# Performance work log

Hardware: AMD Instinct MI355X
Metric: run time of the kernel (lower is better)

The kernel has to match this reference:

```python
import jax, jax.numpy as jnp
import numpy as np
from jax import lax

RESO = 64
PAD = 0.1
PLANES = ('xz', 'xy', 'yz')
_AX = {'xz': (0, 2), 'xy': (0, 1), 'yz': (1, 2)}


def _normalize(p, plane):
    a, b = _AX[plane]
    xy = jnp.stack([p[..., a], p[..., b]], axis=-1)
    xy = (xy + 0.5) / (1.0 + PAD + 1e-6)
    return jnp.clip(xy, 0.0, 1.0 - 1e-6)


def _coord2index(xy):
    xi = (xy * RESO).astype(jnp.int32)
    return xi[..., 0] + RESO * xi[..., 1]  # [B,N]


def _scatter_mean(feat, idx):  # feat [B,N,C], idx [B,N] -> [B,RESO^2,C]
    R2 = RESO * RESO
    def one(f, i):
        s = jnp.zeros((R2, f.shape[-1]), f.dtype).at[i].add(f)
        cnt = jnp.zeros((R2,), f.dtype).at[i].add(1.0)
        return s / jnp.maximum(cnt, 1.0)[:, None]
    return jax.vmap(one)(feat, idx)


def _resblock(x, W0, b0, W1, b1, Ws):
    h = jax.nn.relu(x @ W0.T + b0)
    dx = jax.nn.relu(h @ W1.T + b1)
    return x @ Ws.T + dx


def _conv(x, W, b):
    y = lax.conv_general_dilated(x, W, (1, 1), 'SAME', dimension_numbers=('NCHW', 'OIHW', 'NCHW'))
    return y + b[None, :, None, None]


def _grid_sample_border(fea, grid):
    # fea [B,C,H,W], grid [B,N,2] with (x->W, y->H) in [-1,1]; bilinear, border padding, align_corners=False
    B, C, H, W = fea.shape
    x = jnp.clip(((grid[..., 0] + 1.0) * W - 1.0) * 0.5, 0.0, W - 1.0)
    y = jnp.clip(((grid[..., 1] + 1.0) * H - 1.0) * 0.5, 0.0, H - 1.0)
    x0 = jnp.floor(x); y0 = jnp.floor(y)
    wx = (x - x0)[:, None, :]; wy = (y - y0)[:, None, :]
    x0i = x0.astype(jnp.int32); y0i = y0.astype(jnp.int32)
    x1i = jnp.minimum(x0i + 1, W - 1); y1i = jnp.minimum(y0i + 1, H - 1)
    flat = fea.reshape(B, C, H * W)
    g = lambda yi, xi: jnp.take_along_axis(flat, (yi * W + xi)[:, None, :], axis=2)  # [B,C,N]
    return (g(y0i, x0i) * (1 - wx) * (1 - wy) + g(y0i, x1i) * wx * (1 - wy)
            + g(y1i, x0i) * (1 - wx) * wy + g(y1i, x1i) * wx * wy)


def setup_inputs() -> dict:
    key = jax.random.key(0)
    ks = jax.random.split(key, 16)
    B, N, Nq, H, F = 4, 30000, 30000, 64, 256
    nrm = lambda k, sh, s: jax.random.normal(k, sh, jnp.float32) * s
    return {
        'p': jax.random.uniform(ks[0], (B, N, 3), jnp.float32, -0.5, 0.5),
        'query': jax.random.uniform(ks[1], (B, Nq, 3), jnp.float32, 0.0, 1.0),
        'fc_pos_W': nrm(ks[2], (2 * H, 3), 0.3),
        'fc_pos_b': jnp.zeros((2 * H,), jnp.float32),
        'blk_fc0_W': nrm(ks[3], (3, H, 2 * H), 0.08),
        'blk_fc0_b': jnp.zeros((3, H), jnp.float32),
        'blk_fc1_W': nrm(ks[4], (3, H, H), 0.1),
        'blk_fc1_b': jnp.zeros((3, H), jnp.float32),
        'blk_sc_W': nrm(ks[5], (3, H, 2 * H), 0.08),
        'fc_c_W': nrm(ks[6], (F, H), 0.1),
        'fc_c_b': jnp.zeros((F,), jnp.float32),
        'conv1_W': nrm(ks[7], (F, F, 3, 3), 0.02),
        'conv1_b': jnp.zeros((F,), jnp.float32),
        'conv2_W': nrm(ks[8], (F, F, 3, 3), 0.02),
        'conv2_b': jnp.zeros((F,), jnp.float32),
    }


def reference(p, query, fc_pos_W, fc_pos_b, blk_fc0_W, blk_fc0_b, blk_fc1_W, blk_fc1_b, blk_sc_W, fc_c_W, fc_c_b, conv1_W, conv1_b, conv2_W, conv2_b):
    # point-wise MLP with local pooling (scatter_mean to xz bins, gather back)
    net = p @ fc_pos_W.T + fc_pos_b                  # [B,N,2H]
    net = _resblock(net, blk_fc0_W[0], blk_fc0_b[0], blk_fc1_W[0], blk_fc1_b[0], blk_sc_W[0])  # [B,N,H]
    idx_xz = _coord2index(_normalize(p, 'xz'))       # [B,N]
    for i in (1, 2):
        binmean = _scatter_mean(net, idx_xz)         # [B,R2,H]
        pooled = jnp.take_along_axis(binmean, idx_xz[..., None], axis=1)  # [B,N,H]
        net = jnp.concatenate([net, pooled], axis=-1)
        net = _resblock(net, blk_fc0_W[i], blk_fc0_b[i], blk_fc1_W[i], blk_fc1_b[i], blk_sc_W[i])
    c = net @ fc_c_W.T + fc_c_b                      # [B,N,F]

    B = p.shape[0]
    F = fc_c_W.shape[0]
    out = 0.0
    for plane in PLANES:
        idx = _coord2index(_normalize(p, plane))
        fea = _scatter_mean(c, idx)                  # [B,R2,F]
        fea = fea.transpose(0, 2, 1).reshape(B, F, RESO, RESO)  # H axis = coord1, W axis = coord0
        fea = jax.nn.relu(_conv(fea, conv1_W, conv1_b))
        fea = jax.nn.relu(_conv(fea, conv2_W, conv2_b))
        a, b = _AX[plane]
        grid = jnp.stack([query[..., a], query[..., b]], axis=-1) * 2.0 - 1.0
        out = out + _grid_sample_border(fea, grid)   # [B,F,Nq]
    return out.transpose(0, 2, 1)                    # [B,Nq,F]
```

## Files before the change

### kernel.cpp

```cpp
#include <hip/hip_runtime.h>

#define NPTS 30000
#define PSTR 30208
#define BB 4
#define R2 4096
#define NIMG 12

typedef __attribute__((ext_vector_type(8))) short short8;
typedef __attribute__((ext_vector_type(4))) float floatx4;

__device__ __forceinline__ ushort f2bf(float x){
    union { float f; unsigned u; } v; v.f = x;
    unsigned r = (v.u + 0x7fffu + ((v.u >> 16) & 1u)) >> 16;
    return (ushort)r;
}
__device__ __forceinline__ float bf2f(ushort u){
    union { unsigned u; float f; } v; v.u = ((unsigned)u) << 16; return v.f;
}
__device__ __forceinline__ int p64i(int k){ return (k & 3)*16 + (k >> 2); }

__device__ __forceinline__ int coord_bin(float v){
    float t = (v + 0.5f) / 1.100001f;
    t = fminf(fmaxf(t, 0.0f), 0.999999f);
    return (int)(t * 64.0f);
}

__device__ __forceinline__ void gl_lds16(const ushort* g, ushort* l){
    __builtin_amdgcn_global_load_lds(
        (const __attribute__((address_space(1))) void*)g,
        (__attribute__((address_space(3))) void*)l, 16, 0, 0);
}

__global__ void k_prep(const float* __restrict__ fc_pos_W, const float* __restrict__ fc_pos_b,
                       const float* __restrict__ blk0W, const float* __restrict__ blk1W,
                       const float* __restrict__ blkSW, const float* __restrict__ fccW,
                       const float* __restrict__ c1W, const float* __restrict__ c2W,
                       float* __restrict__ WposTp, float* __restrict__ bposP,
                       ushort* __restrict__ Wcat, ushort* __restrict__ W1p,
                       ushort* __restrict__ Wcp,
                       ushort* __restrict__ WB1, ushort* __restrict__ WB2){
    int t = blockIdx.x*256 + threadIdx.x;
    if (t < 384){ int d = t/128, s = t%128;
        int j = (s<64)? p64i(s) : 64 + p64i(s-64);
        WposTp[t] = fc_pos_W[j*3 + d]; return; }
    t -= 384;
    if (t < 128){ int j = (t<64)? p64i(t) : 64 + p64i(t-64);
        bposP[t] = fc_pos_b[j]; return; }
    t -= 128;
    if (t < 49152){
        int i = t/16384, r = t%16384, n = r/128, kp = r%128;
        int ci = (kp<64)? p64i(kp) : 64 + p64i(kp-64);
        float v = (n<64)? blk0W[(i*64+n)*128 + ci] : blkSW[(i*64+(n-64))*128 + ci];
        Wcat[t] = f2bf(v); return; }
    t -= 49152;
    if (t < 12288){
        int i = t/4096, r = t%4096, n = r/64, kp = r%64;
        W1p[t] = f2bf(blk1W[(i*64+n)*64 + p64i(kp)]); return; }
    t -= 12288;
    if (t < 16384){
        int n = t/64, kp = t%64;
        Wcp[t] = f2bf(fccW[n*64 + p64i(kp)]); return; }
    t -= 16384;
    if (t < 589824){
        int e = t & 7; int rest = t >> 3; int ko = rest & 255; int g5 = rest >> 8;
        int qq = g5 & 3; int kc = (g5 >> 2) & 1; int cc = (g5 >> 3) & 3; int tap = g5 >> 5;
        int kp = cc*64 + kc*32 + qq*8 + e;
        int ci = 64*(kp>>6) + p64i(kp & 63);
        WB1[t] = f2bf(c1W[(ko*256+ci)*9 + tap]); return; }
    t -= 589824;
    if (t < 589824){
        int e = t & 7; int rest = t >> 3; int ko = rest & 255; int g5 = rest >> 8;
        int qq = g5 & 3; int kc = (g5 >> 2) & 1; int cc = (g5 >> 3) & 3; int tap = g5 >> 5;
        int kp = cc*64 + kc*32 + qq*8 + e;
        WB2[t] = f2bf(c2W[(ko*256+kp)*9 + tap]); return; }
}

__global__ void k_net0(const float* __restrict__ p, const float* __restrict__ WposTp,
                       const float* __restrict__ bposP,
                       ushort* __restrict__ NET0, int* __restrict__ IDX){
    int pt = blockIdx.x*256 + threadIdx.x;
    int b = blockIdx.y;
    if (pt >= NPTS) return;
    const float* pp = p + ((long)b*NPTS + pt)*3;
    float p0 = pp[0], p1 = pp[1], p2 = pp[2];
    int c0 = coord_bin(p0), c1 = coord_bin(p1), c2 = coord_bin(p2);
    IDX[(0*BB + b)*NPTS + pt] = c0 + 64*c2;
    IDX[(1*BB + b)*NPTS + pt] = c0 + 64*c1;
    IDX[(2*BB + b)*NPTS + pt] = c1 + 64*c2;
    ushort* out = NET0 + ((long)b*PSTR + pt)*128;
    #pragma unroll
    for (int s = 0; s < 128; s += 4){
        ushort4 v;
        v.x = f2bf(bposP[s+0] + p0*WposTp[s+0] + p1*WposTp[128+s+0] + p2*WposTp[256+s+0]);
        v.y = f2bf(bposP[s+1] + p0*WposTp[s+1] + p1*WposTp[128+s+1] + p2*WposTp[256+s+1]);
        v.z = f2bf(bposP[s+2] + p0*WposTp[s+2] + p1*WposTp[128+s+2] + p2*WposTp[256+s+2]);
        v.w = f2bf(bposP[s+3] + p0*WposTp[s+3] + p1*WposTp[128+s+3] + p2*WposTp[256+s+3]);
        *(ushort4*)(out + s) = v;
    }
}

__global__ void k_qbin(const float* __restrict__ query, int* __restrict__ qIDX){
    int t = blockIdx.x*256 + threadIdx.x;
    if (t >= BB*NPTS) return;
    const float* qp = query + (long)t*3;
    int x = min((int)(fmaxf(qp[0], 0.0f)*16.0f), 15);
    int y = min((int)(fmaxf(qp[1], 0.0f)*16.0f), 15);
    int z = min((int)(fmaxf(qp[2], 0.0f)*16.0f), 15);
    qIDX[t] = (x<<8) | (y<<4) | z;
}

__global__ void k_hist(const int* __restrict__ IDX, int* __restrict__ hist, int n){
    int t = blockIdx.x*256 + threadIdx.x;
    if (t >= n) return;
    int img = t / NPTS;
    atomicAdd(&hist[img*R2 + IDX[t]], 1);
}

__global__ void k_scan(const int* __restrict__ hist, int* __restrict__ binStart,
                       int* __restrict__ cursor){
    __shared__ int sums[256];
    int img = blockIdx.x; int tid = threadIdx.x;
    int v[16]; int s = 0;
    const int* h = hist + img*R2 + tid*16;
    #pragma unroll
    for (int i=0;i<16;i++){ v[i] = s; s += h[i]; }
    sums[tid] = s;
    __syncthreads();
    for (int d=1; d<256; d<<=1){
        int t = (tid>=d)? sums[tid-d] : 0;
        __syncthreads();
        sums[tid] += t;
        __syncthreads();
    }
    int base = (tid==0)? 0 : sums[tid-1];
    int* bs = binStart + img*R2 + tid*16;
    int* cu = cursor  + img*R2 + tid*16;
    #pragma unroll
    for (int i=0;i<16;i++){ bs[i] = base + v[i]; cu[i] = base + v[i]; }
}

__global__ void k_mklist(const int* __restrict__ IDX, int* __restrict__ cursor,
                         int* __restrict__ plist, int n){
    int t = blockIdx.x*256 + threadIdx.x;
    if (t >= n) return;
    int img = t / NPTS; int pt = t - img*NPTS;
    int bin = IDX[t];
    int pos = atomicAdd(&cursor[img*R2 + bin], 1);
    plist[img*NPTS + pos] = pt;
}

__global__ void __launch_bounds__(256) k_res_mfma(
        const ushort* __restrict__ X1, const ushort* __restrict__ X2, int s1, int s2,
        const ushort* __restrict__ Wcat, const float* __restrict__ b0,
        const ushort* __restrict__ W1p, const float* __restrict__ b1,
        ushort* __restrict__ Y){
    __shared__ __align__(16) ushort lds[4][64*72];
    int tid = threadIdx.x, lane = tid & 63, w = tid >> 6;
    int m16 = lane & 15, q = lane >> 4;
    int b = blockIdx.y;
    int pt0 = blockIdx.x*256 + w*64;
    const ushort* x1 = X1 + (long)b*PSTR*s1;
    const ushort* x2 = X2 + (long)b*PSTR*s2;
    floatx4 accH[4][4], accS[4][4];
    #pragma unroll
    for (int nt=0; nt<4; nt++){
        float bv = b0[nt*16 + m16];
        #pragma unroll
        for (int mt=0; mt<4; mt++){
            floatx4 t = {bv,bv,bv,bv}; accH[mt][nt] = t;
            floatx4 z = {0.f,0.f,0.f,0.f}; accS[mt][nt] = z;
        }
    }
    #pragma unroll
    for (int kk=0; kk<4; kk++){
        const ushort* xs = (kk<2)? x1 : x2;
        int st = (kk<2)? s1 : s2;
        int off = (kk&1)*32 + q*8;
        short8 a[4], bh[4], bs[4];
        #pragma unroll
        for (int mt=0; mt<4; mt++)
            a[mt] = *(const short8*)(xs + (long)(pt0 + mt*16 + m16)*st + off);
        #pragma unroll
        for (int nt=0; nt<4; nt++){
            bh[nt] = *(const short8*)(Wcat + (nt*16 + m16)*128 + kk*32 + q*8);
            bs[nt] = *(const short8*)(Wcat + ((nt+4)*16 + m16)*128 + kk*32 + q*8);
        }
        #pragma unroll
        for (int mt=0; mt<4; mt++)
            #pragma unroll
            for (int nt=0; nt<4; nt++){
                accH[mt][nt] = __builtin_amdgcn_mfma_f32_16x16x32_bf16(a[mt], bh[nt], accH[mt][nt], 0,0,0);
                accS[mt][nt] = __builtin_amdgcn_mfma_f32_16x16x32_bf16(a[mt], bs[nt], accS[mt][nt], 0,0,0);
            }
    }
    ushort* myl = lds[w];
    #pragma unroll
    for (int mt=0; mt<4; mt++)
        #pragma unroll
        for (int r=0; r<4; r++){
            int ptl = mt*16 + q*4 + r;
            ushort4 hv;
            hv.x = f2bf(fmaxf(accH[mt][0][r], 0.0f));
            hv.y = f2bf(fmaxf(accH[mt][1][r], 0.0f));
            hv.z = f2bf(fmaxf(accH[mt][2][r], 0.0f));
            hv.w = f2bf(fmaxf(accH[mt][3][r], 0.0f));
            *(ushort4*)&myl[ptl*72 + m16*4] = hv;
        }
    floatx4 accD[4][4];
    #pragma unroll
    for (int nt=0; nt<4; nt++){
        float bv = b1[nt*16 + m16];
        #pragma unroll
        for (int mt=0; mt<4; mt++){ floatx4 t = {bv,bv,bv,bv}; accD[mt][nt] = t; }
    }
    #pragma unroll
    for (int kk=0; kk<2; kk++){
        short8 a[4], bb[4];
        #pragma unroll
        for (int mt=0; mt<4; mt++)
            a[mt] = *(const short8*)&myl[(mt*16 + m16)*72 + kk*32 + q*8];
        #pragma unroll
        for (int nt=0; nt<4; nt++)
            bb[nt] = *(const short8*)(W1p + (nt*16 + m16)*64 + kk*32 + q*8);
        #pragma unroll
        for (int mt=0; mt<4; mt++)
            #pragma unroll
            for (int nt=0; nt<4; nt++)
                accD[mt][nt] = __builtin_amdgcn_mfma_f32_16x16x32_bf16(a[mt], bb[nt], accD[mt][nt], 0,0,0);
    }
    #pragma unroll
    for (int mt=0; mt<4; mt++)
        #pragma unroll
        for (int r=0; r<4; r++){
            int pt = pt0 + mt*16 + q*4 + r;
            if (pt < NPTS){
                ushort4 yv;
                yv.x = f2bf(accS[mt][0][r] + fmaxf(accD[mt][0][r], 0.0f));
                yv.y = f2bf(accS[mt][1][r] + fmaxf(accD[mt][1][r], 0.0f));
                yv.z = f2bf(accS[mt][2][r] + fmaxf(accD[mt][2][r], 0.0f));
                yv.w = f2bf(accS[mt][3][r] + fmaxf(accD[mt][3][r], 0.0f));
                *(ushort4*)(Y + ((long)b*PSTR + pt)*64 + m16*4) = yv;
            }
        }
}

__global__ void k_poolgather(const ushort* __restrict__ Y, const int* __restrict__ plist,
                             const int* __restrict__ binStart, const int* __restrict__ hist,
                             ushort* __restrict__ POOL){
    int tid = threadIdx.x; int lane = tid & 63; int wv = tid >> 6;
    int g = blockIdx.x*4 + wv;
    int b = g >> 12; int bl = g & 4095;
    int idx = b*R2 + bl;
    int start = binStart[idx]; int cnt = hist[idx];
    const int* pl = plist + b*NPTS;
    float s = 0.0f;
    for (int i=0;i<cnt;i++){
        int pt = pl[start+i];
        s += bf2f(Y[((long)b*PSTR + pt)*64 + lane]);
    }
    ushort sv = f2bf(s / fmaxf((float)cnt, 1.0f));
    for (int i=0;i<cnt;i++){
        int pt = pl[start+i];
        POOL[((long)b*PSTR + pt)*64 + lane] = sv;
    }
}

__global__ void __launch_bounds__(256) k_fc_c_mfma(const ushort* __restrict__ X,
        const ushort* __restrict__ Wcp, const float* __restrict__ bc, ushort* __restrict__ C){
    int tid = threadIdx.x, lane = tid & 63, w = tid >> 6;
    int m16 = lane & 15, q = lane >> 4;
    int b = blockIdx.y;
    int pt0 = blockIdx.x*64;
    int n0 = w*64;
    const ushort* xb = X + (long)b*PSTR*64;
    floatx4 acc[4][4];
    #pragma unroll
    for (int nt=0; nt<4; nt++){
        float bv = bc[n0 + nt*16 + m16];
        #pragma unroll
        for (int mt=0; mt<4; mt++){ floatx4 t = {bv,bv,bv,bv}; acc[mt][nt] = t; }
    }
    #pragma unroll
    for (int kk=0; kk<2; kk++){
        short8 a[4], bb[4];
        #pragma unroll
        for (int mt=0; mt<4; mt++)
            a[mt] = *(const short8*)(xb + (long)(pt0 + mt*16 + m16)*64 + kk*32 + q*8);
        #pragma unroll
        for (int nt=0; nt<4; nt++)
            bb[nt] = *(const short8*)(Wcp + (n0 + nt*16 + m16)*64 + kk*32 + q*8);
        #pragma unroll
        for (int mt=0; mt<4; mt++)
            #pragma unroll
            for (int nt=0; nt<4; nt++)
                acc[mt][nt] = __builtin_amdgcn_mfma_f32_16x16x32_bf16(a[mt], bb[nt], acc[mt][nt], 0,0,0);
    }
    #pragma unroll
    for (int mt=0; mt<4; mt++)
        #pragma unroll
        for (int r=0; r<4; r++){
            int pt = pt0 + mt*16 + q*4 + r;
            if (pt < NPTS){
                ushort4 v;
                v.x = f2bf(acc[mt][0][r]); v.y = f2bf(acc[mt][1][r]);
                v.z = f2bf(acc[mt][2][r]); v.w = f2bf(acc[mt][3][r]);
                *(ushort4*)(C + ((long)b*PSTR + pt)*256 + n0 + m16*4) = v;
            }
        }
}

__global__ void k_gatherC(const ushort* __restrict__ C, const int* __restrict__ plist,
                          const int* __restrict__ binStart, const int* __restrict__ hist,
                          ushort* __restrict__ G){
    int tid = threadIdx.x; int lane = tid & 63; int wv = tid >> 6;
    int g = blockIdx.x*4 + wv;
    int img = g >> 12; int bl = g & 4095;
    int b = img & 3;
    int idx = img*R2 + bl;
    int start = binStart[idx]; int cnt = hist[idx];
    const int* pl = plist + img*NPTS;
    float4 acc = {0.f,0.f,0.f,0.f};
    const ushort* Cb = C + (long)b*PSTR*256 + lane*4;
    for (int i=0;i<cnt;i++){
        int pt = pl[start+i];
        ushort4 v = *(const ushort4*)(Cb + (long)pt*256);
        acc.x += bf2f(v.x); acc.y += bf2f(v.y); acc.z += bf2f(v.z); acc.w += bf2f(v.w);
    }
    float inv = 1.0f / fmaxf((float)cnt, 1.0f);
    ushort4 o;
    o.x = f2bf(acc.x*inv); o.y = f2bf(acc.y*inv);
    o.z = f2bf(acc.z*inv); o.w = f2bf(acc.w*inv);
    *(ushort4*)(G + ((long)img*R2 + bl)*256 + lane*4) = o;
}

__global__ void __launch_bounds__(256, 3) k_conv_mfma(const ushort* __restrict__ IN,
        const ushort* __restrict__ WBt, const float* __restrict__ bias, ushort* __restrict__ OUT){
    __shared__ __align__(16) ushort lds[2][3*66*64];
    int tid = threadIdx.x;
    int lane = tid & 63;
    int w = tid >> 6;
    int n0 = __builtin_amdgcn_readfirstlane(w * 64);
    int bid = blockIdx.x;
    int wg = (bid & 7) * 96 + (bid >> 3);
    int img = wg >> 6;
    int y = wg & 63;
    const ushort* inb = IN + (long)img*4096*256;
    int m16 = lane & 15, q = lane >> 4;

    if (tid < 96){
        int st = tid & 7; int c = tid >> 3;
        int buf = c / 6; int rr = (c % 6) >> 1; int colh = (c & 1) * 65;
        short8 z = {0,0,0,0,0,0,0,0};
        *(short8*)&lds[buf][(rr*66 + colh)*64 + st*8] = z;
    }

    floatx4 acc[4][4];
    #pragma unroll
    for (int j=0;j<4;j++){
        float bv = bias[n0 + 16*j + m16];
        #pragma unroll
        for (int i=0;i<4;i++){ floatx4 t = {bv,bv,bv,bv}; acc[i][j] = t; }
    }

    int sgx = lane >> 3;
    int sst = lane & 7;
    int sg  = sst ^ ((1 + sgx) & 7);

    auto stage = [&](int buf, int cc){
        #pragma unroll
        for (int r3 = 0; r3 < 3; ++r3){
            int gy = y + r3 - 1;
            if (gy < 0 || gy > 63) continue;
            const ushort* grow = inb + (long)gy*64*256 + cc*64 + sg*8;
            #pragma unroll
            for (int t = 0; t < 2; ++t){
                int col8 = w + t*4;
                const ushort* gp = grow + (long)(col8*8 + sgx)*256;
                ushort* lp = &lds[buf][(r3*66 + 1 + col8*8)*64];
                gl_lds16(gp, lp);
            }
        }
    };

    auto compute = [&](int buf, int cc){
        const ushort* lb = &lds[buf][0];
        #pragma unroll
        for (int r3 = 0; r3 < 3; ++r3){
            int gy = y + r3 - 1;
            if (gy < 0 || gy > 63) continue;
            #pragma unroll
            for (int s = 0; s < 3; ++s){
                int tap = r3*3 + s;
                #pragma unroll
                for (int kc = 0; kc < 2; ++kc){
                    short8 a[4], b[4];
                    #pragma unroll
                    for (int j=0;j<4;j++)
                        b[j] = *(const short8*)(WBt + (long)(tap*32 + cc*8 + kc*4 + q)*2048
                                                    + (n0 + 16*j + m16)*8);
                    #pragma unroll
                    for (int i=0;i<4;i++){
                        int colh = 16*i + m16 + s;
                        int sl = (kc*4 + q) ^ (colh & 7);
                        a[i] = *(const short8*)(lb + (r3*66 + colh)*64 + sl*8);
                    }
                    #pragma unroll
                    for (int i=0;i<4;i++)
                        #pragma unroll
                        for (int j=0;j<4;j++)
                            acc[i][j] = __builtin_amdgcn_mfma_f32_16x16x32_bf16(a[i], b[j], acc[i][j], 0, 0, 0);
                }
            }
        }
    };

    stage(0, 0);
    __syncthreads();
    #pragma unroll 1
    for (int cc = 0; cc < 4; ++cc){
        if (cc < 3) stage((cc+1)&1, cc+1);
        compute(cc&1, cc);
        __syncthreads();
    }

    long base = ((long)img*4096 + (long)y*64);
    #pragma unroll
    for (int i=0;i<4;i++){
        #pragma unroll
        for (int rr=0;rr<4;rr++){
            int px = 16*i + q*4 + rr;
            long rowoff = (base + px)*256;
            #pragma unroll
            for (int j=0;j<4;j++){
                float v = fmaxf(acc[i][j][rr], 0.0f);
                OUT[rowoff + n0 + 16*j + m16] = f2bf(v);
            }
        }
    }
}

__global__ void k_sample(const ushort* __restrict__ A2, const float* __restrict__ query,
                         const int* __restrict__ qlist, float* __restrict__ out){
    int lane = threadIdx.x & 63;
    int g = blockIdx.x*4 + (threadIdx.x >> 6);
    int b = blockIdx.y;
    int q = qlist[b*NPTS + g];
    const float* qp = query + ((long)b*NPTS + q)*3;
    float q0 = qp[0], q1 = qp[1], q2 = qp[2];
    float a0 = 0.f, a1 = 0.f, a2v = 0.f, a3 = 0.f;
    #pragma unroll
    for (int pl = 0; pl < 3; pl++){
        float qa = (pl==2) ? q1 : q0;
        float qb = (pl==1) ? q1 : q2;
        float gx = qa*2.0f - 1.0f, gy = qb*2.0f - 1.0f;
        float xf = ((gx + 1.0f)*64.0f - 1.0f)*0.5f;
        float yf = ((gy + 1.0f)*64.0f - 1.0f)*0.5f;
        xf = fminf(fmaxf(xf, 0.0f), 63.0f);
        yf = fminf(fmaxf(yf, 0.0f), 63.0f);
        float x0f = floorf(xf), y0f = floorf(yf);
        float wx = xf - x0f, wy = yf - y0f;
        int x0 = (int)x0f, y0 = (int)y0f;
        int x1 = min(x0+1, 63), y1 = min(y0+1, 63);
        const ushort* base = A2 + ((long)(pl*BB+b)*R2)*256 + lane*4;
        ushort4 t00 = *(const ushort4*)(base + (long)(y0*64+x0)*256);
        ushort4 t01 = *(const ushort4*)(base + (long)(y0*64+x1)*256);
        ushort4 t10 = *(const ushort4*)(base + (long)(y1*64+x0)*256);
        ushort4 t11 = *(const ushort4*)(base + (long)(y1*64+x1)*256);
        float w00 = (1.0f-wx)*(1.0f-wy), w01 = wx*(1.0f-wy);
        float w10 = (1.0f-wx)*wy,        w11 = wx*wy;
        a0  += bf2f(t00.x)*w00 + bf2f(t01.x)*w01 + bf2f(t10.x)*w10 + bf2f(t11.x)*w11;
        a1  += bf2f(t00.y)*w00 + bf2f(t01.y)*w01 + bf2f(t10.y)*w10 + bf2f(t11.y)*w11;
        a2v += bf2f(t00.z)*w00 + bf2f(t01.z)*w01 + bf2f(t10.z)*w10 + bf2f(t11.z)*w11;
        a3  += bf2f(t00.w)*w00 + bf2f(t01.w)*w01 + bf2f(t10.w)*w10 + bf2f(t11.w)*w11;
    }
    float4 r; r.x = a0; r.y = a1; r.z = a2v; r.w = a3;
    *(float4*)(out + ((long)b*NPTS + q)*256 + lane*4) = r;
}

extern "C" void kernel_launch(void* const* d_in, const int* in_sizes, int n_in,
                              void* d_out, int out_size, void* d_ws, size_t ws_size,
                              hipStream_t stream){
    (void)in_sizes; (void)n_in; (void)out_size; (void)ws_size;
    const float* p        = (const float*)d_in[0];
    const float* query    = (const float*)d_in[1];
    const float* fc_pos_W = (const float*)d_in[2];
    const float* fc_pos_b = (const float*)d_in[3];
    const float* blk0W    = (const float*)d_in[4];
    const float* blk0b    = (const float*)d_in[5];
    const float* blk1W    = (const float*)d_in[6];
    const float* blk1b    = (const float*)d_in[7];
    const float* blkSW    = (const float*)d_in[8];
    const float* fccW     = (const float*)d_in[9];
    const float* fccB     = (const float*)d_in[10];
    const float* c1W      = (const float*)d_in[11];
    const float* c1b      = (const float*)d_in[12];
    const float* c2W      = (const float*)d_in[13];
    const float* c2b      = (const float*)d_in[14];

    char* ws = (char*)d_ws;
    size_t off = 0;
    auto alloc = [&](size_t bytes)->char*{
        char* r = ws + off; off = (off + bytes + 255) & ~(size_t)255; return r; };
    float* WposTp = (float*)alloc(384*4);
    float* bposP  = (float*)alloc(128*4);
    ushort* Wcat  = (ushort*)alloc(49152UL*2);
    ushort* W1p   = (ushort*)alloc(12288UL*2);
    ushort* Wcp   = (ushort*)alloc(16384UL*2);
    ushort* WB1   = (ushort*)alloc(589824UL*2);
    ushort* WB2   = (ushort*)alloc(589824UL*2);
    int*   IDX   = (int*)  alloc((size_t)NIMG*NPTS*4);
    int*   qIDX  = (int*)  alloc((size_t)BB*NPTS*4);
    int*   hist  = (int*)  alloc((size_t)(NIMG+BB)*R2*4);
    int*   qhist = hist + (size_t)NIMG*R2;
    int*   binStart = (int*)alloc((size_t)NIMG*R2*4);
    int*   cursor   = (int*)alloc((size_t)NIMG*R2*4);
    int*   plist    = (int*)alloc((size_t)NIMG*NPTS*4);
    int*   qbinStart = (int*)alloc((size_t)BB*R2*4);
    int*   qcursor   = (int*)alloc((size_t)BB*R2*4);
    int*   qlist     = (int*)alloc((size_t)BB*NPTS*4);
    ushort* NET0 = (ushort*)alloc((size_t)BB*PSTR*128*2);
    ushort* Ya   = (ushort*)alloc((size_t)BB*PSTR*64*2);
    ushort* Yb   = (ushort*)alloc((size_t)BB*PSTR*64*2);
    ushort* POOL = (ushort*)alloc((size_t)BB*PSTR*64*2);
    ushort* C    = (ushort*)alloc((size_t)BB*PSTR*256*2);
    ushort* G    = (ushort*)alloc(12582912UL*2);
    ushort* A1   = (ushort*)alloc(12582912UL*2);
    ushort* A2   = (ushort*)alloc(12582912UL*2);

    dim3 blk(256);
    k_prep<<<4914, blk, 0, stream>>>(fc_pos_W, fc_pos_b, blk0W, blk1W, blkSW, fccW, c1W, c2W,
                                     WposTp, bposP, Wcat, W1p, Wcp, WB1, WB2);
    k_net0<<<dim3(118, BB), blk, 0, stream>>>(p, WposTp, bposP, NET0, IDX);
    k_qbin<<<(BB*NPTS + 255)/256, blk, 0, stream>>>(query, qIDX);
    hipMemsetAsync(hist, 0, (size_t)(NIMG+BB)*R2*4, stream);
    k_hist  <<<(NIMG*NPTS + 255)/256, blk, 0, stream>>>(IDX, hist, NIMG*NPTS);
    k_hist  <<<(BB*NPTS + 255)/256, blk, 0, stream>>>(qIDX, qhist, BB*NPTS);
    k_scan  <<<NIMG, blk, 0, stream>>>(hist, binStart, cursor);
    k_scan  <<<BB,   blk, 0, stream>>>(qhist, qbinStart, qcursor);
    k_mklist<<<(NIMG*NPTS + 255)/256, blk, 0, stream>>>(IDX, cursor, plist, NIMG*NPTS);
    k_mklist<<<(BB*NPTS + 255)/256, blk, 0, stream>>>(qIDX, qcursor, qlist, BB*NPTS);
    k_res_mfma<<<dim3(118,BB), blk, 0, stream>>>(NET0, NET0 + 64, 128, 128,
                                                 Wcat, blk0b, W1p, blk1b, Ya);
    k_poolgather<<<4096, blk, 0, stream>>>(Ya, plist, binStart, hist, POOL);
    k_res_mfma<<<dim3(118,BB), blk, 0, stream>>>(Ya, POOL, 64, 64,
                                                 Wcat + 16384, blk0b + 64, W1p + 4096, blk1b + 64, Yb);
    k_poolgather<<<4096, blk, 0, stream>>>(Yb, plist, binStart, hist, POOL);
    k_res_mfma<<<dim3(118,BB), blk, 0, stream>>>(Yb, POOL, 64, 64,
                                                 Wcat + 32768, blk0b + 128, W1p + 8192, blk1b + 128, Ya);
    k_fc_c_mfma<<<dim3(469,BB), blk, 0, stream>>>(Ya, Wcp, fccB, C);
    k_gatherC<<<12288, blk, 0, stream>>>(C, plist, binStart, hist, G);
    k_conv_mfma<<<dim3(768), blk, 0, stream>>>(G,  WB1, c1b, A1);
    k_conv_mfma<<<dim3(768), blk, 0, stream>>>(A1, WB2, c2b, A2);
    k_sample<<<dim3(7500,BB), blk, 0, stream>>>(A2, query, qlist, (float*)d_out);
}
```

Before: 548.5 us.

## Scatter-mean 64-wide features before the fc_c linear layer instead of after

Because fc_c is affine, the mean of fc_c(x) over a bin equals fc_c of the mean of x for non-empty bins. The change gathers and averages the 64-channel features per bin first, then runs the 64->256 MFMA GEMM on the 12x4096 bin rows, zeroing empty bins. This drops the per-point 256-wide C buffer and its write and gather traffic. It adds a small GEMM over 49k rows and changes bf16 rounding order slightly.

```diff
diff --git a/kernel.cpp b/kernel.cpp
--- a/kernel.cpp
+++ b/kernel.cpp
@@ -265,53 +265,9 @@
     }
 }
 
-__global__ void __launch_bounds__(256) k_fc_c_mfma(const ushort* __restrict__ X,
-        const ushort* __restrict__ Wcp, const float* __restrict__ bc, ushort* __restrict__ C){
-    int tid = threadIdx.x, lane = tid & 63, w = tid >> 6;
-    int m16 = lane & 15, q = lane >> 4;
-    int b = blockIdx.y;
-    int pt0 = blockIdx.x*64;
-    int n0 = w*64;
-    const ushort* xb = X + (long)b*PSTR*64;
-    floatx4 acc[4][4];
-    #pragma unroll
-    for (int nt=0; nt<4; nt++){
-        float bv = bc[n0 + nt*16 + m16];
-        #pragma unroll
-        for (int mt=0; mt<4; mt++){ floatx4 t = {bv,bv,bv,bv}; acc[mt][nt] = t; }
-    }
-    #pragma unroll
-    for (int kk=0; kk<2; kk++){
-        short8 a[4], bb[4];
-        #pragma unroll
-        for (int mt=0; mt<4; mt++)
-            a[mt] = *(const short8*)(xb + (long)(pt0 + mt*16 + m16)*64 + kk*32 + q*8);
-        #pragma unroll
-        for (int nt=0; nt<4; nt++)
-            bb[nt] = *(const short8*)(Wcp + (n0 + nt*16 + m16)*64 + kk*32 + q*8);
-        #pragma unroll
-        for (int mt=0; mt<4; mt++)
-            #pragma unroll
-            for (int nt=0; nt<4; nt++)
-                acc[mt][nt] = __builtin_amdgcn_mfma_f32_16x16x32_bf16(a[mt], bb[nt], acc[mt][nt], 0,0,0);
-    }
-    #pragma unroll
-    for (int mt=0; mt<4; mt++)
-        #pragma unroll
-        for (int r=0; r<4; r++){
-            int pt = pt0 + mt*16 + q*4 + r;
-            if (pt < NPTS){
-                ushort4 v;
-                v.x = f2bf(acc[mt][0][r]); v.y = f2bf(acc[mt][1][r]);
-                v.z = f2bf(acc[mt][2][r]); v.w = f2bf(acc[mt][3][r]);
-                *(ushort4*)(C + ((long)b*PSTR + pt)*256 + n0 + m16*4) = v;
-            }
-        }
-}
-
-__global__ void k_gatherC(const ushort* __restrict__ C, const int* __restrict__ plist,
-                          const int* __restrict__ binStart, const int* __restrict__ hist,
-                          ushort* __restrict__ G){
+__global__ void k_gather64(const ushort* __restrict__ Y, const int* __restrict__ plist,
+                           const int* __restrict__ binStart, const int* __restrict__ hist,
+                           ushort* __restrict__ BIN){
     int tid = threadIdx.x; int lane = tid & 63; int wv = tid >> 6;
     int g = blockIdx.x*4 + wv;
     int img = g >> 12; int bl = g & 4095;
@@ -319,18 +275,59 @@
     int idx = img*R2 + bl;
     int start = binStart[idx]; int cnt = hist[idx];
     const int* pl = plist + img*NPTS;
-    float4 acc = {0.f,0.f,0.f,0.f};
-    const ushort* Cb = C + (long)b*PSTR*256 + lane*4;
+    const ushort* Yb = Y + (long)b*PSTR*64 + lane;
+    float s = 0.0f;
     for (int i=0;i<cnt;i++){
         int pt = pl[start+i];
-        ushort4 v = *(const ushort4*)(Cb + (long)pt*256);
-        acc.x += bf2f(v.x); acc.y += bf2f(v.y); acc.z += bf2f(v.z); acc.w += bf2f(v.w);
-    }
-    float inv = 1.0f / fmaxf((float)cnt, 1.0f);
-    ushort4 o;
-    o.x = f2bf(acc.x*inv); o.y = f2bf(acc.y*inv);
-    o.z = f2bf(acc.z*inv); o.w = f2bf(acc.w*inv);
-    *(ushort4*)(G + ((long)img*R2 + bl)*256 + lane*4) = o;
+        s += bf2f(Yb[(long)pt*64]);
+    }
+    BIN[(long)g*64 + lane] = f2bf(s / fmaxf((float)cnt, 1.0f));
+}
+
+__global__ void __launch_bounds__(256) k_fc_bins(const ushort* __restrict__ BIN,
+        const ushort* __restrict__ Wcp, const float* __restrict__ bc,
+        const int* __restrict__ hist, ushort* __restrict__ G){
+    int tid = threadIdx.x, lane = tid & 63, w = tid >> 6;
+    int m16 = lane & 15, q = lane >> 4;
+    int r0 = blockIdx.x*64;
+    int n0 = w*64;
+    floatx4 acc[4][4];
+    #pragma unroll
+    for (int nt=0; nt<4; nt++){
+        float bv = bc[n0 + nt*16 + m16];
+        #pragma unroll
+        for (int mt=0; mt<4; mt++){ floatx4 t = {bv,bv,bv,bv}; acc[mt][nt] = t; }
+    }
+    #pragma unroll
+    for (int kk=0; kk<2; kk++){
+        short8 a[4], bb[4];
+        #pragma unroll
+        for (int mt=0; mt<4; mt++)
+            a[mt] = *(const short8*)(BIN + (long)(r0 + mt*16 + m16)*64 + kk*32 + q*8);
+        #pragma unroll
+        for (int nt=0; nt<4; nt++)
+            bb[nt] = *(const short8*)(Wcp + (n0 + nt*16 + m16)*64 + kk*32 + q*8);
+        #pragma unroll
+        for (int mt=0; mt<4; mt++)
+            #pragma unroll
+            for (int nt=0; nt<4; nt++)
+                acc[mt][nt] = __builtin_amdgcn_mfma_f32_16x16x32_bf16(a[mt], bb[nt], acc[mt][nt], 0,0,0);
+    }
+    #pragma unroll
+    for (int mt=0; mt<4; mt++)
+        #pragma unroll
+        for (int r=0; r<4; r++){
+            int row = r0 + mt*16 + q*4 + r;
+            int cnt = hist[row];
+            ushort4 v;
+            if (cnt > 0){
+                v.x = f2bf(acc[mt][0][r]); v.y = f2bf(acc[mt][1][r]);
+                v.z = f2bf(acc[mt][2][r]); v.w = f2bf(acc[mt][3][r]);
+            } else {
+                v.x = 0; v.y = 0; v.z = 0; v.w = 0;
+            }
+            *(ushort4*)(G + (long)row*256 + n0 + m16*4) = v;
+        }
 }
 
 __global__ void __launch_bounds__(256, 3) k_conv_mfma(const ushort* __restrict__ IN,
@@ -522,7 +519,7 @@
     ushort* Ya   = (ushort*)alloc((size_t)BB*PSTR*64*2);
     ushort* Yb   = (ushort*)alloc((size_t)BB*PSTR*64*2);
     ushort* POOL = (ushort*)alloc((size_t)BB*PSTR*64*2);
-    ushort* C    = (ushort*)alloc((size_t)BB*PSTR*256*2);
+    ushort* BIN64= (ushort*)alloc((size_t)NIMG*R2*64*2);
     ushort* G    = (ushort*)alloc(12582912UL*2);
     ushort* A1   = (ushort*)alloc(12582912UL*2);
     ushort* A2   = (ushort*)alloc(12582912UL*2);
@@ -547,8 +544,8 @@
     k_poolgather<<<4096, blk, 0, stream>>>(Yb, plist, binStart, hist, POOL);
     k_res_mfma<<<dim3(118,BB), blk, 0, stream>>>(Yb, POOL, 64, 64,
                                                  Wcat + 32768, blk0b + 128, W1p + 8192, blk1b + 128, Ya);
-    k_fc_c_mfma<<<dim3(469,BB), blk, 0, stream>>>(Ya, Wcp, fccB, C);
-    k_gatherC<<<12288, blk, 0, stream>>>(C, plist, binStart, hist, G);
+    k_gather64<<<12288, blk, 0, stream>>>(Ya, plist, binStart, hist, BIN64);
+    k_fc_bins<<<768, blk, 0, stream>>>(BIN64, Wcp, fccB, hist, G);
     k_conv_mfma<<<dim3(768), blk, 0, stream>>>(G,  WB1, c1b, A1);
     k_conv_mfma<<<dim3(768), blk, 0, stream>>>(A1, WB2, c2b, A2);
     k_sample<<<dim3(7500,BB), blk, 0, stream>>>(A2, query, qlist, (float*)d_out);
```

New measurement: 523.3 us. -4.6%, faster.
